# Performance work log

Hardware: AMD Instinct MI355X
Metric: run time of the kernel (lower is better)

## Reference

```python
import jax, jax.numpy as jnp
import numpy as np

N_NODES = 50000
HEADS = 8
NEG_SLOPE = 0.2


def _gat_conv(x, src, dst, n, W, a_src, a_dst, b, concat):
    # W: [H*C, F_in], a_src/a_dst: [H, C], b: [H*C] or [C]
    H, C = a_src.shape
    h = (x @ W.T).reshape(-1, H, C)                      # [N, H, C]
    al_src = jnp.einsum('nhc,hc->nh', h, a_src)          # [N, H]
    al_dst = jnp.einsum('nhc,hc->nh', h, a_dst)          # [N, H]
    e = jax.nn.leaky_relu(al_src[src] + al_dst[dst], NEG_SLOPE)  # [E, H]
    # segment softmax over incoming edges of each dst node
    m = jax.lax.stop_gradient(jax.ops.segment_max(e, dst, num_segments=n))
    ee = jnp.exp(e - m[dst])
    denom = jax.ops.segment_sum(ee, dst, num_segments=n)
    alpha = ee / denom[dst]                              # [E, H]
    out = jax.ops.segment_sum(alpha[:, :, None] * h[src], dst, num_segments=n)  # [N, H, C]
    out = out.reshape(n, H * C) if concat else out.mean(axis=1)
    return out + b


def setup_inputs() -> dict:
    key = jax.random.key(0)
    ks = jax.random.split(key, 12)
    N, F_in, Hd, H, Ncls = N_NODES, 128, 32, HEADS, 40
    E = 800000
    x = jax.random.normal(ks[0], (N, F_in), dtype=jnp.float32)
    edge_index = jax.random.randint(ks[1], (2, E), 0, N, dtype=jnp.int64)
    s1 = 1.0 / np.sqrt(F_in)
    W1 = jax.random.normal(ks[2], (H * Hd, F_in), dtype=jnp.float32) * s1
    a_src1 = jax.random.normal(ks[3], (H, Hd), dtype=jnp.float32) * 0.1
    a_dst1 = jax.random.normal(ks[4], (H, Hd), dtype=jnp.float32) * 0.1
    b1 = jnp.zeros((H * Hd,), dtype=jnp.float32)
    s2 = 1.0 / np.sqrt(H * Hd)
    W2 = jax.random.normal(ks[5], (H * Ncls, H * Hd), dtype=jnp.float32) * s2
    a_src2 = jax.random.normal(ks[6], (H, Ncls), dtype=jnp.float32) * 0.1
    a_dst2 = jax.random.normal(ks[7], (H, Ncls), dtype=jnp.float32) * 0.1
    b2 = jnp.zeros((Ncls,), dtype=jnp.float32)
    return {"x": x, "edge_index": edge_index,
            "W1": W1, "a_src1": a_src1, "a_dst1": a_dst1, "b1": b1,
            "W2": W2, "a_src2": a_src2, "a_dst2": a_dst2, "b2": b2}


def reference(x, edge_index, W1, a_src1, a_dst1, b1, W2, a_src2, a_dst2, b2):
    n = x.shape[0]
    # PyG GATConv default: add self loops
    loop = jnp.arange(n, dtype=edge_index.dtype)
    src = jnp.concatenate([edge_index[0], loop])
    dst = jnp.concatenate([edge_index[1], loop])
    # layer 1 (concat heads) -> ELU; dropout identity in eval mode
    h = _gat_conv(x, src, dst, n, W1, a_src1, a_dst1, b1, concat=True)
    h = jax.nn.elu(h)
    # layer 2 (mean over heads)
    out = _gat_conv(h, src, dst, n, W2, a_src2, a_dst2, b2, concat=False)
    return jax.nn.log_softmax(out, axis=1)
```

## Files before the change

kernel.cpp:

```cpp
#include <hip/hip_runtime.h>
#include <hip/hip_bf16.h>
#include <math.h>

typedef unsigned short ushort_t;
typedef unsigned char uchar_t;
typedef __attribute__((ext_vector_type(8))) short short8;
typedef __attribute__((ext_vector_type(4))) float f32x4;
typedef __attribute__((ext_vector_type(2))) float f32x2;
typedef __attribute__((ext_vector_type(4))) unsigned short u16x4;

#define LOG2E 1.44269504088896f

static __device__ __forceinline__ float b2f(ushort_t u) {
    union { unsigned int i; float f; } v; v.i = ((unsigned int)u) << 16; return v.f;
}
static __device__ __forceinline__ ushort_t f2b(float f) {
    unsigned int x = __float_as_uint(f);
    unsigned int r = (x + 0x7fffu + ((x >> 16) & 1u)) >> 16;
    return (ushort_t)r;
}
static __device__ __forceinline__ uchar_t f2e4m3(float f) {
    int r = __builtin_amdgcn_cvt_pk_fp8_f32(f, f, 0, false);
    return (uchar_t)(r & 0xff);
}
static __device__ __forceinline__ float exp2fast(float x) {
    return __builtin_amdgcn_exp2f(x);
}


__global__ void conv_kernel(const float* __restrict__ src, ushort_t* __restrict__ dst, int n4) {
    for (int i = blockIdx.x * blockDim.x + threadIdx.x; i < n4; i += gridDim.x * blockDim.x) {
        float4 v = *(const float4*)(src + i * 4);
        u16x4 o = { f2b(v.x), f2b(v.y), f2b(v.z), f2b(v.w) };
        *(u16x4*)(dst + i * 4) = o;
    }
}

template<int K, int Cd>
__global__ void build_wa(const float* __restrict__ W, const float* __restrict__ as,
                         const float* __restrict__ ad, ushort_t* __restrict__ Bext, int rowoff) {
    int tid = blockIdx.x * blockDim.x + threadIdx.x;
    if (tid >= 16 * K) return;
    int col = tid / K, k = tid - col * K;
    const float* a = (col < 8) ? as : ad;
    int h = col & 7;
    float s = 0.f;
    #pragma unroll 4
    for (int c = 0; c < Cd; ++c)
        s += W[(size_t)(h * Cd + c) * K + k] * a[h * Cd + c];
    Bext[(size_t)(rowoff + col) * K + k] = f2b(s * LOG2E);
}

__global__ void pad_row_kernel(float* als1, float* als2, uchar_t* h1f8, uchar_t* h2f8, int n) {
    int t = threadIdx.x;
    if (t < 8) { als1[(size_t)n * 8 + t] = -1e30f; als2[(size_t)n * 8 + t] = -1e30f; }
    if (t < 256) h1f8[(size_t)n * 256 + t] = 0;
    if (t < 320) h2f8[(size_t)n * 320 + t] = 0;
}


__global__ void count_kernel(const int* __restrict__ ei, int E, int n, int* __restrict__ deg) {
    int e = blockIdx.x * blockDim.x + threadIdx.x;
    int Etot = E + n;
    if (e >= Etot) return;
    int dst = (e < E) ? ei[E + e] : (e - E);
    atomicAdd(&deg[dst], 1);
}

__global__ void scan_kernel(const int* __restrict__ deg, int* __restrict__ rowptr,
                            int* __restrict__ cursor, int n) {
    __shared__ int wsum[16];
    int t = threadIdx.x;
    int lane = t & 63, wid = t >> 6;
    int carry = 0;
    for (int base = 0; base < n; base += 1024) {
        int i = base + t;
        int v = (i < n) ? ((deg[i] + 7) & ~7) : 0;
        int val = v;
        #pragma unroll
        for (int off = 1; off < 64; off <<= 1) {
            int nv = __shfl_up(val, off);
            if (lane >= off) val += nv;
        }
        if (lane == 63) wsum[wid] = val;
        __syncthreads();
        int wpre = 0, tot = 0;
        #pragma unroll
        for (int w = 0; w < 16; ++w) {
            int s = wsum[w];
            if (w < wid) wpre += s;
            tot += s;
        }
        int excl = carry + wpre + val - v;
        if (i < n) { rowptr[i] = excl; cursor[i] = excl; }
        carry += tot;
        __syncthreads();
    }
    if (t == 0) rowptr[n] = carry;
}

__global__ void scatter_kernel(const int* __restrict__ ei, int E, int n,
                               int* __restrict__ cursor, int* __restrict__ ssrc) {
    int e = blockIdx.x * blockDim.x + threadIdx.x;
    int Etot = E + n;
    if (e >= Etot) return;
    int src, dst;
    if (e < E) { src = ei[e]; dst = ei[E + e]; }
    else       { src = e - E; dst = e - E; }
    int pos = atomicAdd(&cursor[dst], 1);
    ssrc[pos] = src;
}

__global__ void pad_fill_kernel(const int* __restrict__ rowptr, const int* __restrict__ cursor,
                                int* __restrict__ ssrc, int n) {
    int i = blockIdx.x * blockDim.x + threadIdx.x;
    if (i >= n) return;
    int p = cursor[i], e = rowptr[i + 1];
    for (; p < e; ++p) ssrc[p] = n;
}


template<int NFRAG, int K>
__global__ __launch_bounds__(512) void gemm_lds_al(const ushort_t* __restrict__ A,
                                                   const ushort_t* __restrict__ B,
                                                   uchar_t* __restrict__ C,
                                                   float* __restrict__ als,
                                                   float* __restrict__ ald, int M) {
    constexpr int N = NFRAG * 16;
    constexpr int NOUT = (NFRAG - 1) * 16;
    constexpr int RS = 40;
    constexpr int NK = K / 32;
    __shared__ ushort_t Bs[2][N * RS];
    const int t = threadIdx.x;
    const int w = t >> 6, l = t & 63;
    const int r0 = blockIdx.x * 256 + w * 32;
    int arow0 = r0 + (l & 15);
    int arow1 = r0 + 16 + (l & 15);
    if (arow0 >= M) arow0 = M - 1;
    if (arow1 >= M) arow1 = M - 1;
    const int koff = (l >> 4) * 8;
    const ushort_t* ap0 = A + (size_t)arow0 * K + koff;
    const ushort_t* ap1 = A + (size_t)arow1 * K + koff;

    f32x4 acc0[NFRAG], acc1[NFRAG];
    #pragma unroll
    for (int i = 0; i < NFRAG; ++i) {
        acc0[i] = (f32x4){0.f, 0.f, 0.f, 0.f};
        acc1[i] = (f32x4){0.f, 0.f, 0.f, 0.f};
    }

    auto stage = [&](int buf, int k0) {
        #pragma unroll
        for (int c = t; c < N * 4; c += 512) {
            int row = c >> 2, part = (c & 3) << 3;
            *(short8*)&Bs[buf][row * RS + part] =
                *(const short8*)(B + (size_t)row * K + k0 + part);
        }
    };

    stage(0, 0);
    __syncthreads();
    #pragma unroll
    for (int kk = 0; kk < NK; ++kk) {
        int buf = kk & 1;
        if (kk + 1 < NK) stage(buf ^ 1, (kk + 1) * 32);
        short8 a0 = *(const short8*)(ap0 + kk * 32);
        short8 a1 = *(const short8*)(ap1 + kk * 32);
        #pragma unroll
        for (int nf = 0; nf < NFRAG; ++nf) {
            short8 b = *(const short8*)&Bs[buf][(nf * 16 + (l & 15)) * RS + koff];
            acc0[nf] = __builtin_amdgcn_mfma_f32_16x16x32_bf16(a0, b, acc0[nf], 0, 0, 0);
            acc1[nf] = __builtin_amdgcn_mfma_f32_16x16x32_bf16(a1, b, acc1[nf], 0, 0, 0);
        }
        __syncthreads();
    }

    const int crow0 = r0 + (l >> 4) * 4;
    #pragma unroll
    for (int nf = 0; nf < NFRAG - 1; ++nf) {
        #pragma unroll
        for (int j = 0; j < 4; ++j) {
            int row0 = crow0 + j, row1 = crow0 + 16 + j;
            if (row0 < M) C[(size_t)row0 * NOUT + nf * 16 + (l & 15)] = f2e4m3(acc0[nf][j]);
            if (row1 < M) C[(size_t)row1 * NOUT + nf * 16 + (l & 15)] = f2e4m3(acc1[nf][j]);
        }
    }
    {
        int col = l & 15;
        float* dstp = (col < 8) ? als : ald;
        int h = col & 7;
        #pragma unroll
        for (int j = 0; j < 4; ++j) {
            int row0 = crow0 + j, row1 = crow0 + 16 + j;
            if (row0 < M) dstp[(size_t)row0 * 8 + h] = acc0[NFRAG - 1][j];
            if (row1 < M) dstp[(size_t)row1 * 8 + h] = acc1[NFRAG - 1][j];
        }
    }
}


__device__ __forceinline__ float lrelu(float e) { return (e > 0.f) ? e : 0.2f * e; }

__global__ void agg1_kernel(const uchar_t* __restrict__ h1, const float* __restrict__ als,
                            const float* __restrict__ aldv, const float* __restrict__ b1,
                            const int* __restrict__ rowptr, const int* __restrict__ ssrc,
                            ushort_t* __restrict__ hout, int n) {
    int node = blockIdx.x * 4 + (threadIdx.x >> 6);
    if (node >= n) return;
    int l = threadIdx.x & 63;
    int h = l >> 3;
    float ald = aldv[node * 8 + h];
    int beg = rowptr[node], end = rowptr[node + 1];
    float den = 0.f, a0 = 0.f, a1 = 0.f, a2 = 0.f, a3 = 0.f;
    for (int p = beg; p < end; p += 8) {
        int4 sA = *(const int4*)(ssrc + p);
        int4 sB = *(const int4*)(ssrc + p + 4);
        float w0 = exp2fast(lrelu(als[sA.x * 8 + h] + ald));
        float w1 = exp2fast(lrelu(als[sA.y * 8 + h] + ald));
        float w2 = exp2fast(lrelu(als[sA.z * 8 + h] + ald));
        float w3 = exp2fast(lrelu(als[sA.w * 8 + h] + ald));
        float w4 = exp2fast(lrelu(als[sB.x * 8 + h] + ald));
        float w5 = exp2fast(lrelu(als[sB.y * 8 + h] + ald));
        float w6 = exp2fast(lrelu(als[sB.z * 8 + h] + ald));
        float w7 = exp2fast(lrelu(als[sB.w * 8 + h] + ald));
        int g0 = *(const int*)(h1 + (size_t)sA.x * 256 + l * 4);
        int g1 = *(const int*)(h1 + (size_t)sA.y * 256 + l * 4);
        int g2 = *(const int*)(h1 + (size_t)sA.z * 256 + l * 4);
        int g3 = *(const int*)(h1 + (size_t)sA.w * 256 + l * 4);
        int g4 = *(const int*)(h1 + (size_t)sB.x * 256 + l * 4);
        int g5 = *(const int*)(h1 + (size_t)sB.y * 256 + l * 4);
        int g6 = *(const int*)(h1 + (size_t)sB.z * 256 + l * 4);
        int g7 = *(const int*)(h1 + (size_t)sB.w * 256 + l * 4);
        den += ((w0 + w1) + (w2 + w3)) + ((w4 + w5) + (w6 + w7));
        #define DQ(g, wv) { \
            f32x2 lo = __builtin_amdgcn_cvt_pk_f32_fp8(g, false); \
            f32x2 hi = __builtin_amdgcn_cvt_pk_f32_fp8(g, true);  \
            a0 += wv * lo.x; a1 += wv * lo.y; a2 += wv * hi.x; a3 += wv * hi.y; }
        DQ(g0, w0) DQ(g1, w1) DQ(g2, w2) DQ(g3, w3)
        DQ(g4, w4) DQ(g5, w5) DQ(g6, w6) DQ(g7, w7)
        #undef DQ
    }
    float inv = 1.f / den;
    float4 bv = *(const float4*)(b1 + l * 4);
    float v0 = a0 * inv + bv.x, v1 = a1 * inv + bv.y;
    float v2 = a2 * inv + bv.z, v3 = a3 * inv + bv.w;
    u16x4 o;
    o.x = f2b((v0 > 0.f) ? v0 : __expf(v0) - 1.f);
    o.y = f2b((v1 > 0.f) ? v1 : __expf(v1) - 1.f);
    o.z = f2b((v2 > 0.f) ? v2 : __expf(v2) - 1.f);
    o.w = f2b((v3 > 0.f) ? v3 : __expf(v3) - 1.f);
    *(u16x4*)(hout + (size_t)node * 256 + l * 4) = o;
}


__global__ void agg2_kernel(const uchar_t* __restrict__ h2, const float* __restrict__ als,
                            const float* __restrict__ aldv, const float* __restrict__ b2,
                            const int* __restrict__ rowptr, const int* __restrict__ ssrc,
                            float* __restrict__ out, int n) {
    int node = blockIdx.x * 4 + (threadIdx.x >> 6);
    if (node >= n) return;
    int l = threadIdx.x & 63;
    int li = (l < 40) ? l : 0;
    int hd = li / 5;
    int cg = li - hd * 5;
    float ald = aldv[node * 8 + hd];
    int beg = rowptr[node], end = rowptr[node + 1];
    const uchar_t* base = h2 + hd * 40 + cg * 8;
    float den = 0.f;
    float a0 = 0.f, a1 = 0.f, a2 = 0.f, a3 = 0.f, a4 = 0.f, a5 = 0.f, a6 = 0.f, a7 = 0.f;
    for (int p = beg; p < end; p += 8) {
        int4 sA = *(const int4*)(ssrc + p);
        int4 sB = *(const int4*)(ssrc + p + 4);
        float w0 = exp2fast(lrelu(als[sA.x * 8 + hd] + ald));
        float w1 = exp2fast(lrelu(als[sA.y * 8 + hd] + ald));
        float w2 = exp2fast(lrelu(als[sA.z * 8 + hd] + ald));
        float w3 = exp2fast(lrelu(als[sA.w * 8 + hd] + ald));
        float w4 = exp2fast(lrelu(als[sB.x * 8 + hd] + ald));
        float w5 = exp2fast(lrelu(als[sB.y * 8 + hd] + ald));
        float w6 = exp2fast(lrelu(als[sB.z * 8 + hd] + ald));
        float w7 = exp2fast(lrelu(als[sB.w * 8 + hd] + ald));
        uint2 g0 = *(const uint2*)(base + (size_t)sA.x * 320);
        uint2 g1 = *(const uint2*)(base + (size_t)sA.y * 320);
        uint2 g2 = *(const uint2*)(base + (size_t)sA.z * 320);
        uint2 g3 = *(const uint2*)(base + (size_t)sA.w * 320);
        uint2 g4 = *(const uint2*)(base + (size_t)sB.x * 320);
        uint2 g5 = *(const uint2*)(base + (size_t)sB.y * 320);
        uint2 g6 = *(const uint2*)(base + (size_t)sB.z * 320);
        uint2 g7 = *(const uint2*)(base + (size_t)sB.w * 320);
        den += ((w0 + w1) + (w2 + w3)) + ((w4 + w5) + (w6 + w7));
        #define DQ(g, wv) { \
            f32x2 q0 = __builtin_amdgcn_cvt_pk_f32_fp8((int)g.x, false); \
            f32x2 q1 = __builtin_amdgcn_cvt_pk_f32_fp8((int)g.x, true);  \
            f32x2 q2 = __builtin_amdgcn_cvt_pk_f32_fp8((int)g.y, false); \
            f32x2 q3 = __builtin_amdgcn_cvt_pk_f32_fp8((int)g.y, true);  \
            a0 += wv * q0.x; a1 += wv * q0.y; a2 += wv * q1.x; a3 += wv * q1.y; \
            a4 += wv * q2.x; a5 += wv * q2.y; a6 += wv * q3.x; a7 += wv * q3.y; }
        DQ(g0, w0) DQ(g1, w1) DQ(g2, w2) DQ(g3, w3)
        DQ(g4, w4) DQ(g5, w5) DQ(g6, w6) DQ(g7, w7)
        #undef DQ
    }
    float inv = 1.f / den;
    float v[8] = {a0 * inv, a1 * inv, a2 * inv, a3 * inv,
                  a4 * inv, a5 * inv, a6 * inv, a7 * inv};
    #pragma unroll
    for (int j = 0; j < 8; ++j) {
        float s = v[j];
        s += __shfl_down(s, 20);
        s += __shfl_down(s, 10);
        s += __shfl_down(s, 5);
        v[j] = s;
    }
    if (l < 5) {
        float wv[8];
        #pragma unroll
        for (int j = 0; j < 8; ++j) wv[j] = 0.125f * v[j] + b2[l * 8 + j];
        float m8 = wv[0];
        #pragma unroll
        for (int j = 1; j < 8; ++j) m8 = fmaxf(m8, wv[j]);
        float mx = m8;
        #pragma unroll
        for (int k = 0; k < 5; ++k) mx = fmaxf(mx, __shfl(m8, k));
        float se8 = 0.f;
        #pragma unroll
        for (int j = 0; j < 8; ++j) se8 += __expf(wv[j] - mx);
        float se = 0.f;
        #pragma unroll
        for (int k = 0; k < 5; ++k) se += __shfl(se8, k);
        float lse = mx + __logf(se);
        float* op = out + (size_t)node * 40 + l * 8;
        float4 o0 = {wv[0] - lse, wv[1] - lse, wv[2] - lse, wv[3] - lse};
        float4 o1 = {wv[4] - lse, wv[5] - lse, wv[6] - lse, wv[7] - lse};
        *(float4*)op = o0;
        *(float4*)(op + 4) = o1;
    }
}


extern "C" void kernel_launch(void* const* d_in, const int* in_sizes, int n_in,
                              void* d_out, int out_size, void* d_ws, size_t ws_size,
                              hipStream_t stream) {
    const float* x      = (const float*)d_in[0];
    const int*   ei     = (const int*)d_in[1];
    const float* W1     = (const float*)d_in[2];
    const float* a_src1 = (const float*)d_in[3];
    const float* a_dst1 = (const float*)d_in[4];
    const float* b1     = (const float*)d_in[5];
    const float* W2     = (const float*)d_in[6];
    const float* a_src2 = (const float*)d_in[7];
    const float* a_dst2 = (const float*)d_in[8];
    const float* b2     = (const float*)d_in[9];
    float* out = (float*)d_out;

    const int n    = in_sizes[0] / 128;
    const int E    = in_sizes[1] / 2;
    const int Etot = E + n;
    const int EpM  = Etot + 7 * n + 16;

    char* w = (char*)d_ws;
    auto take = [&](size_t bytes) {
        char* p = w;
        w += (bytes + 255) & ~(size_t)255;
        return p;
    };
    int*      deg    = (int*)take((size_t)n * 4);
    int*      rowptr = (int*)take((size_t)(n + 1) * 4);
    int*      cursor = (int*)take((size_t)n * 4);
    int*      ssrc   = (int*)take((size_t)EpM * 4);
    ushort_t* xb     = (ushort_t*)take((size_t)n * 128 * 2);
    ushort_t* w1b    = (ushort_t*)take((size_t)272 * 128 * 2);
    ushort_t* w2b    = (ushort_t*)take((size_t)336 * 256 * 2);
    uchar_t*  h1f8   = (uchar_t*)take((size_t)(n + 1) * 256);
    ushort_t* helu   = (ushort_t*)take((size_t)n * 256 * 2);
    uchar_t*  h2f8   = (uchar_t*)take((size_t)(n + 1) * 320);
    float*    als1   = (float*)take((size_t)(n + 1) * 8 * 4);
    float*    ald1   = (float*)take((size_t)n * 8 * 4);
    float*    als2   = (float*)take((size_t)(n + 1) * 8 * 4);
    float*    ald2   = (float*)take((size_t)n * 8 * 4);

    hipMemsetAsync(deg, 0, (size_t)n * 4, stream);
    pad_row_kernel<<<1, 512, 0, stream>>>(als1, als2, h1f8, h2f8, n);

    conv_kernel<<<2048, 256, 0, stream>>>(x, xb, n * 128 / 4);
    conv_kernel<<<32, 256, 0, stream>>>(W1, w1b, 256 * 128 / 4);
    conv_kernel<<<80, 256, 0, stream>>>(W2, w2b, 320 * 256 / 4);
    build_wa<128, 32><<<8, 256, 0, stream>>>(W1, a_src1, a_dst1, w1b, 256);
    build_wa<256, 40><<<16, 256, 0, stream>>>(W2, a_src2, a_dst2, w2b, 320);

    int eb = (Etot + 255) / 256;
    count_kernel<<<eb, 256, 0, stream>>>(ei, E, n, deg);
    scan_kernel<<<1, 1024, 0, stream>>>(deg, rowptr, cursor, n);
    scatter_kernel<<<eb, 256, 0, stream>>>(ei, E, n, cursor, ssrc);
    pad_fill_kernel<<<(n + 255) / 256, 256, 0, stream>>>(rowptr, cursor, ssrc, n);

    int gb = (n + 255) / 256;
    int nb4 = (n + 3) / 4;

    gemm_lds_al<17, 128><<<gb, 512, 0, stream>>>(xb, w1b, h1f8, als1, ald1, n);
    agg1_kernel<<<nb4, 256, 0, stream>>>(h1f8, als1, ald1, b1, rowptr, ssrc, helu, n);

    gemm_lds_al<21, 256><<<gb, 512, 0, stream>>>(helu, w2b, h2f8, als2, ald2, n);
    agg2_kernel<<<nb4, 256, 0, stream>>>(h2f8, als2, ald2, b2, rowptr, ssrc, out, n);
}
```

Before: 306.3 us.

## Merge prep kernels into fused launches and halve GEMM rows per block

The separate weight-conversion, attention-vector folding and pad-row kernels become one prep kernel, and the x conversion and degree counting share a single launch, which cuts launch count and serialization. The GEMM now gives each wave 16 rows instead of 32, so blocks cover 128 rows and twice as many blocks are launched. That raises occupancy and parallelism over 50k rows. In exchange, each block's LDS-staged B tile is reused across fewer A rows, and twice as many blocks restage it.

Result: faster. 296.4 us (-3.2%).

```diff
diff --git a/kernel.cpp b/kernel.cpp
--- a/kernel.cpp
+++ b/kernel.cpp
@@ -28,19 +28,10 @@
 }
 
 
-__global__ void conv_kernel(const float* __restrict__ src, ushort_t* __restrict__ dst, int n4) {
-    for (int i = blockIdx.x * blockDim.x + threadIdx.x; i < n4; i += gridDim.x * blockDim.x) {
-        float4 v = *(const float4*)(src + i * 4);
-        u16x4 o = { f2b(v.x), f2b(v.y), f2b(v.z), f2b(v.w) };
-        *(u16x4*)(dst + i * 4) = o;
-    }
-}
-
 template<int K, int Cd>
-__global__ void build_wa(const float* __restrict__ W, const float* __restrict__ as,
-                         const float* __restrict__ ad, ushort_t* __restrict__ Bext, int rowoff) {
-    int tid = blockIdx.x * blockDim.x + threadIdx.x;
-    if (tid >= 16 * K) return;
+static __device__ void wa_item(const float* __restrict__ W, const float* __restrict__ as,
+                               const float* __restrict__ ad, ushort_t* __restrict__ Bext,
+                               int rowoff, int tid) {
     int col = tid / K, k = tid - col * K;
     const float* a = (col < 8) ? as : ad;
     int h = col & 7;
@@ -51,21 +42,58 @@
     Bext[(size_t)(rowoff + col) * K + k] = f2b(s * LOG2E);
 }
 
-__global__ void pad_row_kernel(float* als1, float* als2, uchar_t* h1f8, uchar_t* h2f8, int n) {
-    int t = threadIdx.x;
-    if (t < 8) { als1[(size_t)n * 8 + t] = -1e30f; als2[(size_t)n * 8 + t] = -1e30f; }
-    if (t < 256) h1f8[(size_t)n * 256 + t] = 0;
-    if (t < 320) h2f8[(size_t)n * 320 + t] = 0;
-}
-
-
-__global__ void count_kernel(const int* __restrict__ ei, int E, int n, int* __restrict__ deg) {
-    int e = blockIdx.x * blockDim.x + threadIdx.x;
-    int Etot = E + n;
-    if (e >= Etot) return;
-    int dst = (e < E) ? ei[E + e] : (e - E);
-    atomicAdd(&deg[dst], 1);
-}
+__global__ void prep_kernel(const float* __restrict__ W1, const float* __restrict__ W2,
+                            const float* __restrict__ as1, const float* __restrict__ ad1,
+                            const float* __restrict__ as2, const float* __restrict__ ad2,
+                            ushort_t* __restrict__ w1b, ushort_t* __restrict__ w2b,
+                            float* als1, float* als2, uchar_t* h1f8, uchar_t* h2f8, int n) {
+    int b = blockIdx.x, t = threadIdx.x;
+    if (b < 40) {
+        for (int i = b * 256 + t; i < 8192 + 20480; i += 40 * 256) {
+            if (i < 8192) {
+                float4 v = *(const float4*)(W1 + i * 4);
+                u16x4 o = { f2b(v.x), f2b(v.y), f2b(v.z), f2b(v.w) };
+                *(u16x4*)(w1b + i * 4) = o;
+            } else {
+                int j = i - 8192;
+                float4 v = *(const float4*)(W2 + j * 4);
+                u16x4 o = { f2b(v.x), f2b(v.y), f2b(v.z), f2b(v.w) };
+                *(u16x4*)(w2b + j * 4) = o;
+            }
+        }
+    } else if (b < 64) {
+        for (int i = (b - 40) * 256 + t; i < 2048 + 4096; i += 24 * 256) {
+            if (i < 2048) wa_item<128, 32>(W1, as1, ad1, w1b, 256, i);
+            else          wa_item<256, 40>(W2, as2, ad2, w2b, 320, i - 2048);
+        }
+    } else {
+        if (t < 8) { als1[(size_t)n * 8 + t] = -1e30f; als2[(size_t)n * 8 + t] = -1e30f; }
+        h1f8[(size_t)n * 256 + t] = 0;
+        h2f8[(size_t)n * 320 + t] = 0;
+        if (t < 64) h2f8[(size_t)n * 320 + 256 + t] = 0;
+    }
+}
+
+
+__global__ void convx_count_kernel(const float* __restrict__ x, ushort_t* __restrict__ xb, int n4x,
+                                   const int* __restrict__ ei, int E, int n, int* __restrict__ deg) {
+    int b = blockIdx.x, t = threadIdx.x;
+    if (b < 2048) {
+        for (int i = b * 256 + t; i < n4x; i += 2048 * 256) {
+            float4 v = *(const float4*)(x + i * 4);
+            u16x4 o = { f2b(v.x), f2b(v.y), f2b(v.z), f2b(v.w) };
+            *(u16x4*)(xb + i * 4) = o;
+        }
+    } else {
+        int e = (b - 2048) * 256 + t;
+        int Etot = E + n;
+        if (e < Etot) {
+            int dst = (e < E) ? ei[E + e] : (e - E);
+            atomicAdd(&deg[dst], 1);
+        }
+    }
+}
+
 
 __global__ void scan_kernel(const int* __restrict__ deg, int* __restrict__ rowptr,
                             int* __restrict__ cursor, int n) {
@@ -133,21 +161,15 @@
     __shared__ ushort_t Bs[2][N * RS];
     const int t = threadIdx.x;
     const int w = t >> 6, l = t & 63;
-    const int r0 = blockIdx.x * 256 + w * 32;
-    int arow0 = r0 + (l & 15);
-    int arow1 = r0 + 16 + (l & 15);
-    if (arow0 >= M) arow0 = M - 1;
-    if (arow1 >= M) arow1 = M - 1;
+    const int r0 = blockIdx.x * 128 + w * 16;
+    int arow = r0 + (l & 15);
+    if (arow >= M) arow = M - 1;
     const int koff = (l >> 4) * 8;
-    const ushort_t* ap0 = A + (size_t)arow0 * K + koff;
-    const ushort_t* ap1 = A + (size_t)arow1 * K + koff;
-
-    f32x4 acc0[NFRAG], acc1[NFRAG];
+    const ushort_t* ap = A + (size_t)arow * K + koff;
+
+    f32x4 acc[NFRAG];
     #pragma unroll
-    for (int i = 0; i < NFRAG; ++i) {
-        acc0[i] = (f32x4){0.f, 0.f, 0.f, 0.f};
-        acc1[i] = (f32x4){0.f, 0.f, 0.f, 0.f};
-    }
+    for (int i = 0; i < NFRAG; ++i) acc[i] = (f32x4){0.f, 0.f, 0.f, 0.f};
 
     auto stage = [&](int buf, int k0) {
         #pragma unroll
@@ -164,13 +186,11 @@
     for (int kk = 0; kk < NK; ++kk) {
         int buf = kk & 1;
         if (kk + 1 < NK) stage(buf ^ 1, (kk + 1) * 32);
-        short8 a0 = *(const short8*)(ap0 + kk * 32);
-        short8 a1 = *(const short8*)(ap1 + kk * 32);
+        short8 a = *(const short8*)(ap + kk * 32);
         #pragma unroll
         for (int nf = 0; nf < NFRAG; ++nf) {
             short8 b = *(const short8*)&Bs[buf][(nf * 16 + (l & 15)) * RS + koff];
-            acc0[nf] = __builtin_amdgcn_mfma_f32_16x16x32_bf16(a0, b, acc0[nf], 0, 0, 0);
-            acc1[nf] = __builtin_amdgcn_mfma_f32_16x16x32_bf16(a1, b, acc1[nf], 0, 0, 0);
+            acc[nf] = __builtin_amdgcn_mfma_f32_16x16x32_bf16(a, b, acc[nf], 0, 0, 0);
         }
         __syncthreads();
     }
@@ -180,9 +200,8 @@
     for (int nf = 0; nf < NFRAG - 1; ++nf) {
         #pragma unroll
         for (int j = 0; j < 4; ++j) {
-            int row0 = crow0 + j, row1 = crow0 + 16 + j;
-            if (row0 < M) C[(size_t)row0 * NOUT + nf * 16 + (l & 15)] = f2e4m3(acc0[nf][j]);
-            if (row1 < M) C[(size_t)row1 * NOUT + nf * 16 + (l & 15)] = f2e4m3(acc1[nf][j]);
+            int row = crow0 + j;
+            if (row < M) C[(size_t)row * NOUT + nf * 16 + (l & 15)] = f2e4m3(acc[nf][j]);
         }
     }
     {
@@ -191,9 +210,8 @@
         int h = col & 7;
         #pragma unroll
         for (int j = 0; j < 4; ++j) {
-            int row0 = crow0 + j, row1 = crow0 + 16 + j;
-            if (row0 < M) dstp[(size_t)row0 * 8 + h] = acc0[NFRAG - 1][j];
-            if (row1 < M) dstp[(size_t)row1 * 8 + h] = acc1[NFRAG - 1][j];
+            int row = crow0 + j;
+            if (row < M) dstp[(size_t)row * 8 + h] = acc[NFRAG - 1][j];
         }
     }
 }
@@ -378,21 +396,17 @@
     float*    ald2   = (float*)take((size_t)n * 8 * 4);
 
     hipMemsetAsync(deg, 0, (size_t)n * 4, stream);
-    pad_row_kernel<<<1, 512, 0, stream>>>(als1, als2, h1f8, h2f8, n);
-
-    conv_kernel<<<2048, 256, 0, stream>>>(x, xb, n * 128 / 4);
-    conv_kernel<<<32, 256, 0, stream>>>(W1, w1b, 256 * 128 / 4);
-    conv_kernel<<<80, 256, 0, stream>>>(W2, w2b, 320 * 256 / 4);
-    build_wa<128, 32><<<8, 256, 0, stream>>>(W1, a_src1, a_dst1, w1b, 256);
-    build_wa<256, 40><<<16, 256, 0, stream>>>(W2, a_src2, a_dst2, w2b, 320);
+
+    prep_kernel<<<65, 256, 0, stream>>>(W1, W2, a_src1, a_dst1, a_src2, a_dst2,
+                                        w1b, w2b, als1, als2, h1f8, h2f8, n);
 
     int eb = (Etot + 255) / 256;
-    count_kernel<<<eb, 256, 0, stream>>>(ei, E, n, deg);
+    convx_count_kernel<<<2048 + eb, 256, 0, stream>>>(x, xb, n * 128 / 4, ei, E, n, deg);
     scan_kernel<<<1, 1024, 0, stream>>>(deg, rowptr, cursor, n);
     scatter_kernel<<<eb, 256, 0, stream>>>(ei, E, n, cursor, ssrc);
     pad_fill_kernel<<<(n + 255) / 256, 256, 0, stream>>>(rowptr, cursor, ssrc, n);
 
-    int gb = (n + 255) / 256;
+    int gb = (n + 127) / 128;
     int nb4 = (n + 3) / 4;
 
     gemm_lds_al<17, 128><<<gb, 512, 0, stream>>>(xb, w1b, h1f8, als1, ald1, n);
```
